# Optimization experiments

Measured on AMD Instinct MI355X. Metric: run time of the kernel, lower is better.

Reference implementation:

```python
import jax, jax.numpy as jnp
import numpy as np

B, L, D, M_MAX = 4, 4096, 1024, 512


def setup_inputs() -> dict:
    key = jax.random.key(0)
    k_ct, k_enc, k_lo, k_hi, k_w = jax.random.split(key, 5)
    concept_tokens = jax.random.normal(k_ct, (B, M_MAX, D), dtype=jnp.float32)
    encoder_out = jax.random.normal(k_enc, (B, L, D), dtype=jnp.float32)
    # sorted unique boundary positions per batch, first boundary at position 0
    rng = np.random.RandomState(0)
    idx = np.stack([np.sort(rng.choice(np.arange(1, L), size=M_MAX - 1, replace=False)) for _ in range(B)])
    boundary_idx = jnp.asarray(np.concatenate([np.zeros((B, 1), dtype=np.int64), idx], axis=1))  # [B, M_max]
    # probs < 0.5 everywhere except at boundary positions (>= 0.5), so cumsum(mask)-1 < M_max
    lo = jax.random.uniform(k_lo, (B, L), minval=0.02, maxval=0.48)
    hi = jax.random.uniform(k_hi, (B, M_MAX), minval=0.5, maxval=1.0)
    rows = jnp.arange(B)[:, None]
    boundary_probs = lo.at[rows, boundary_idx].set(hi)
    concept_mask = jnp.ones((B, M_MAX), dtype=bool)
    W = jax.random.normal(k_w, (D, D), dtype=jnp.float32) * 0.02  # residual_proj.weight (out = x @ W.T)
    return {"concept_tokens": concept_tokens, "encoder_out": encoder_out,
            "boundary_probs": boundary_probs, "boundary_idx": boundary_idx,
            "concept_mask": concept_mask, "W": W}


def _ema_smooth(concept_tokens, p_at_bounds):
    """h_i = (1-p_i)*h_{i-1} + p_i*c_i via associative scan; h_0 = c_0."""
    h0 = concept_tokens[:, 0]                                  # [B, d]
    p_rest = p_at_bounds[:, 1:]                                # [B, M-1]
    decay = jnp.clip(1.0 - p_rest, 1e-7, None)
    b = p_rest[..., None] * concept_tokens[:, 1:]              # [B, M-1, d]
    a = jnp.broadcast_to(decay[..., None], b.shape)

    def combine(x, y):
        a1, b1 = x
        a2, b2 = y
        return a1 * a2, a2 * b1 + b2

    A, Bc = jax.lax.associative_scan(combine, (a, b), axis=1)
    h_rest = A * h0[:, None, :] + Bc                           # h_i = A_i*h0 + B_i
    return jnp.concatenate([h0[:, None, :], h_rest], axis=1)   # [B, M, d]


def reference(concept_tokens, encoder_out, boundary_probs, boundary_idx, concept_mask, W):
    d = encoder_out.shape[-1]
    # Eq.5: EMA over concept tokens with boundary probs gathered at boundary positions
    p_raw = jnp.take_along_axis(boundary_probs, boundary_idx, axis=1)          # [B, M]
    p_at_bounds = jnp.where(concept_mask, p_raw, 1.0)
    p_at_bounds = jnp.clip(p_at_bounds, 0.1, None)
    smoothed = _ema_smooth(concept_tokens, p_at_bounds)                        # [B, M, d]
    # Eq.8: plug-back via running boundary count
    boundary_mask = boundary_probs >= 0.5                                      # [B, L]
    plug_back_idx = jnp.clip(jnp.cumsum(boundary_mask.astype(jnp.int32), axis=1) - 1, 0, None)
    plugback = jnp.take_along_axis(smoothed, plug_back_idx[..., None], axis=1)  # [B, L, d]
    # Eq.6/7/9: confidence + STE (forward value is exactly 1.0)
    b_f = boundary_mask.astype(boundary_probs.dtype)
    c_t = b_f * boundary_probs + (1.0 - b_f) * (1.0 - boundary_probs)
    ste_c = c_t + jax.lax.stop_gradient(1.0 - c_t)
    upsampled = ste_c[..., None] * plugback
    # Eq.3: residual linear (no bias)
    return upsampled + jnp.einsum('bld,ed->ble', encoder_out, W)
```

## Files before the change

kernel.cpp:

```cpp
#include <hip/hip_runtime.h>
#include <hip/hip_bf16.h>
#include <stdint.h>


#define B_  4
#define L_  4096
#define D_  1024
#define M_  512

typedef __attribute__((ext_vector_type(8))) short bf16x8;
typedef __attribute__((ext_vector_type(4))) float f32x4;
typedef __attribute__((ext_vector_type(8))) unsigned short u16x8;

__device__ inline unsigned short f2bf(float f) {
    unsigned u = __float_as_uint(f);
    u += 0x7fffu + ((u >> 16) & 1u);
    return (unsigned short)(u >> 16);
}

__global__ void prep_kernel(const float* __restrict__ enc, const float* __restrict__ W,
                            const float* __restrict__ probs,
                            unsigned short* __restrict__ encb, unsigned short* __restrict__ Wb,
                            int* __restrict__ pbi) {
    __shared__ int part[256];
    int blk = blockIdx.x;
    int tid = threadIdx.x;
    if (blk < 8704) {
        const float* src; unsigned short* dst; int i;
        if (blk < 8192) { src = enc; dst = encb; i = blk * 256 + tid; }
        else            { src = W;   dst = Wb;   i = (blk - 8192) * 256 + tid; }
        float4 x0 = ((const float4*)src)[2 * i];
        float4 x1 = ((const float4*)src)[2 * i + 1];
        u16x8 v;
        v[0] = f2bf(x0.x); v[1] = f2bf(x0.y); v[2] = f2bf(x0.z); v[3] = f2bf(x0.w);
        v[4] = f2bf(x1.x); v[5] = f2bf(x1.y); v[6] = f2bf(x1.z); v[7] = f2bf(x1.w);
        ((u16x8*)dst)[i] = v;
    } else {
        int b = blk - 8704;
        const float4* pr = (const float4*)(probs + b * L_);
        int cnt[16]; int s = 0;
        #pragma unroll
        for (int u = 0; u < 4; ++u) {
            float4 x = pr[tid * 4 + u];
            s += (x.x >= 0.5f); cnt[u * 4 + 0] = s;
            s += (x.y >= 0.5f); cnt[u * 4 + 1] = s;
            s += (x.z >= 0.5f); cnt[u * 4 + 2] = s;
            s += (x.w >= 0.5f); cnt[u * 4 + 3] = s;
        }
        part[tid] = s;
        __syncthreads();
        for (int off = 1; off < 256; off <<= 1) {
            int x = part[tid];
            int y = (tid >= off) ? part[tid - off] : 0;
            __syncthreads();
            part[tid] = x + y;
            __syncthreads();
        }
        int excl = part[tid] - s;
        int4* po = (int4*)(pbi + b * L_ + tid * 16);
        #pragma unroll
        for (int u = 0; u < 4; ++u) {
            int4 o;
            o.x = max(excl + cnt[u * 4 + 0] - 1, 0);
            o.y = max(excl + cnt[u * 4 + 1] - 1, 0);
            o.z = max(excl + cnt[u * 4 + 2] - 1, 0);
            o.w = max(excl + cnt[u * 4 + 3] - 1, 0);
            po[u] = o;
        }
    }
}

__global__ void ema1_kernel(const float* __restrict__ ct, const float* __restrict__ probs,
                            const int* __restrict__ bidx, float2* __restrict__ summ) {
    int b = blockIdx.z, ch = blockIdx.y;
    int d = blockIdx.x * 256 + threadIdx.x;
    __shared__ float pa[64], pb[64];
    if (threadIdx.x < 64) {
        int m = ch * 64 + threadIdx.x;
        int idx = bidx[b * M_ + m];
        float pv = fmaxf(probs[b * L_ + idx], 0.1f);
        pa[threadIdx.x] = (m == 0) ? 0.0f : fmaxf(1.0f - pv, 1e-7f);
        pb[threadIdx.x] = (m == 0) ? 1.0f : pv;
    }
    __syncthreads();
    const float* ctp = ct + ((size_t)b * M_ + ch * 64) * D_ + d;
    float A = 1.0f, Bv = 0.0f;
    #pragma unroll 8
    for (int i = 0; i < 64; ++i) {
        float c = ctp[(size_t)i * D_];
        A  = pa[i] * A;
        Bv = pa[i] * Bv + pb[i] * c;
    }
    summ[((size_t)b * 8 + ch) * D_ + d] = make_float2(A, Bv);
}

__global__ void ema2_kernel(const float* __restrict__ ct, const float* __restrict__ probs,
                            const int* __restrict__ bidx, const float2* __restrict__ summ,
                            float* __restrict__ smoothed) {
    int b = blockIdx.z, ch = blockIdx.y;
    int d = blockIdx.x * 256 + threadIdx.x;
    __shared__ float pa[64], pb[64];
    if (threadIdx.x < 64) {
        int m = ch * 64 + threadIdx.x;
        int idx = bidx[b * M_ + m];
        float pv = fmaxf(probs[b * L_ + idx], 0.1f);
        pa[threadIdx.x] = (m == 0) ? 0.0f : fmaxf(1.0f - pv, 1e-7f);
        pb[threadIdx.x] = (m == 0) ? 1.0f : pv;
    }
    __syncthreads();
    float h = 0.0f;
    for (int c = 0; c < ch; ++c) {
        float2 s2 = summ[((size_t)b * 8 + c) * D_ + d];
        h = s2.x * h + s2.y;
    }
    const float* ctp = ct + ((size_t)b * M_ + ch * 64) * D_ + d;
    float*       smp = smoothed + ((size_t)b * M_ + ch * 64) * D_ + d;
    #pragma unroll 8
    for (int i = 0; i < 64; ++i) {
        float c = ctp[(size_t)i * D_];
        h = pa[i] * h + pb[i] * c;
        smp[(size_t)i * D_] = h;
    }
}

#define NT_ 32

__global__ __launch_bounds__(512, 1) void gemm3_kernel(
    const unsigned short* __restrict__ encb, const unsigned short* __restrict__ Wb,
    const float* __restrict__ smoothed, const int* __restrict__ pbi,
    float* __restrict__ out)
{
    __shared__ __align__(16) unsigned short As[3][256 * 32];
    __shared__ __align__(16) unsigned short Bs[3][256 * 32];

    const int tid  = threadIdx.x;
    const int lane = tid & 63;
    const int w    = tid >> 6;
    const int wm   = w >> 2;
    const int wn   = w & 3;
    const int l15  = lane & 15;
    const int l16  = lane >> 4;

    const int orig = blockIdx.x;
    const int rm   = (orig & 7) * 32 + (orig >> 3);
    const size_t rowBase = (size_t)(rm >> 2) * 256;
    const int    colBase = (rm & 3) * 256;

    const int rsw = (((lane & 3) ^ ((lane >> 2) & 3)) << 3);

#define STAGE(kt, s)                                                                     \
  {                                                                                      \
    _Pragma("unroll")                                                                    \
    for (int i_ = 0; i_ < 2; ++i_) {                                                     \
      int row_ = i_ * 128 + w * 16 + (lane >> 2);                                        \
      const unsigned short* ga_ = encb + (rowBase + row_) * D_ + (kt) * 32 + rsw;        \
      __builtin_amdgcn_global_load_lds(                                                  \
          (const __attribute__((address_space(1))) void*)ga_,                            \
          (__attribute__((address_space(3))) void*)&As[s][i_ * 4096 + w * 512], 16, 0, 0);\
      const unsigned short* gb_ = Wb + (size_t)(colBase + row_) * D_ + (kt) * 32 + rsw;  \
      __builtin_amdgcn_global_load_lds(                                                  \
          (const __attribute__((address_space(1))) void*)gb_,                            \
          (__attribute__((address_space(3))) void*)&Bs[s][i_ * 4096 + w * 512], 16, 0, 0);\
    }                                                                                    \
  }

    f32x4 acc[8][4] = {};

    STAGE(0, 0);
    STAGE(1, 1);
    asm volatile("s_waitcnt vmcnt(4)" ::: "memory");
    __builtin_amdgcn_s_barrier();
    __builtin_amdgcn_sched_barrier(0);

    int s = 0;
    for (int t = 0; t < NT_; ++t) {
        const char* aB = (const char*)As[s];
        const char* bB = (const char*)Bs[s];
        const int swz = (l15 & 3) << 4;
        bf16x8 a[8], bb[4];
        #pragma unroll
        for (int m = 0; m < 8; ++m)
            a[m] = *(const bf16x8*)(aB + (wm * 128 + m * 16 + l15) * 64 + ((l16 * 16) ^ swz));
        #pragma unroll
        for (int n = 0; n < 4; ++n)
            bb[n] = *(const bf16x8*)(bB + (wn * 64 + n * 16 + l15) * 64 + ((l16 * 16) ^ swz));

        int s2 = s + 2; if (s2 >= 3) s2 -= 3;
        if (t + 2 < NT_) STAGE(t + 2, s2);

        __builtin_amdgcn_s_setprio(1);
        #pragma unroll
        for (int m = 0; m < 8; ++m)
            #pragma unroll
            for (int n = 0; n < 4; ++n)
                acc[m][n] = __builtin_amdgcn_mfma_f32_16x16x32_bf16(a[m], bb[n], acc[m][n], 0, 0, 0);
        __builtin_amdgcn_s_setprio(0);

        if (t + 1 < NT_) {
            if (t + 2 < NT_) { asm volatile("s_waitcnt vmcnt(4)" ::: "memory"); }
            else             { asm volatile("s_waitcnt vmcnt(0)" ::: "memory"); }
            __builtin_amdgcn_s_barrier();
            __builtin_amdgcn_sched_barrier(0);
        }
        s += 1; if (s >= 3) s -= 3;
    }
#undef STAGE

    #pragma unroll
    for (int m = 0; m < 8; ++m) {
        const size_t row0 = rowBase + wm * 128 + m * 16;
        #pragma unroll
        for (int j = 0; j < 4; ++j) {
            size_t row = row0 + l16 * 4 + j;
            int b  = (int)(row >> 12);
            int pb = pbi[row];
            pb = pb < (M_ - 1) ? pb : (M_ - 1);
            const float* sm = smoothed + ((size_t)(b * M_ + pb)) * D_;
            #pragma unroll
            for (int n = 0; n < 4; ++n) {
                int col = colBase + wn * 64 + n * 16 + l15;
                out[row * D_ + col] = acc[m][n][j] + sm[col];
            }
        }
    }
}

#define LDP 72
__global__ __launch_bounds__(256, 2) void gemm_fused_kernel(
    const float* __restrict__ enc, const unsigned short* __restrict__ Wb,
    const float* __restrict__ smoothed, const int* __restrict__ pbi,
    float* __restrict__ out)
{
    __shared__ unsigned short Asf[128][LDP];
    __shared__ unsigned short Bsf[128][LDP];
    const int tid  = threadIdx.x;
    const int lane = tid & 63;
    const int wid  = tid >> 6;
    const int wm   = wid >> 1;
    const int wn   = wid & 1;
    const int l15  = lane & 15;
    const int l16  = lane >> 4;
    const size_t rowBase = (size_t)blockIdx.x * 128;
    const int    colBase = blockIdx.y * 128;
    f32x4 acc[4][4] = {};
    for (int t = 0; t < D_ / 64; ++t) {
        const int k0 = t * 64;
        #pragma unroll
        for (int i = 0; i < 4; ++i) {
            int c = i * 256 + tid;
            int r = c >> 3;
            int c8 = c & 7;
            const float4* g = (const float4*)(enc + (rowBase + r) * D_ + k0 + c8 * 8);
            float4 x0 = g[0];
            float4 x1 = g[1];
            u16x8 v;
            v[0] = f2bf(x0.x); v[1] = f2bf(x0.y); v[2] = f2bf(x0.z); v[3] = f2bf(x0.w);
            v[4] = f2bf(x1.x); v[5] = f2bf(x1.y); v[6] = f2bf(x1.z); v[7] = f2bf(x1.w);
            *(u16x8*)&Asf[r][c8 * 8] = v;
        }
        #pragma unroll
        for (int i = 0; i < 4; ++i) {
            int c = i * 256 + tid;
            int r = c >> 3;
            int c8 = c & 7;
            u16x8 v = *(const u16x8*)(Wb + (size_t)(colBase + r) * D_ + k0 + c8 * 8);
            *(u16x8*)&Bsf[r][c8 * 8] = v;
        }
        __syncthreads();
        #pragma unroll
        for (int kk = 0; kk < 2; ++kk) {
            bf16x8 a[4], bbf[4];
            #pragma unroll
            for (int m = 0; m < 4; ++m)
                a[m] = *(const bf16x8*)&Asf[wm * 64 + m * 16 + l15][kk * 32 + l16 * 8];
            #pragma unroll
            for (int n = 0; n < 4; ++n)
                bbf[n] = *(const bf16x8*)&Bsf[wn * 64 + n * 16 + l15][kk * 32 + l16 * 8];
            #pragma unroll
            for (int m = 0; m < 4; ++m)
                #pragma unroll
                for (int n = 0; n < 4; ++n)
                    acc[m][n] = __builtin_amdgcn_mfma_f32_16x16x32_bf16(a[m], bbf[n], acc[m][n], 0, 0, 0);
        }
        __syncthreads();
    }
    #pragma unroll
    for (int m = 0; m < 4; ++m) {
        #pragma unroll
        for (int j = 0; j < 4; ++j) {
            size_t row = rowBase + wm * 64 + m * 16 + l16 * 4 + j;
            int b  = (int)(row >> 12);
            int pb = pbi[row];
            pb = pb < (M_ - 1) ? pb : (M_ - 1);
            const float* sm = smoothed + ((size_t)(b * M_ + pb)) * D_;
            #pragma unroll
            for (int n = 0; n < 4; ++n) {
                int col = colBase + wn * 64 + n * 16 + l15;
                out[row * D_ + col] = acc[m][n][j] + sm[col];
            }
        }
    }
}

extern "C" void kernel_launch(void* const* d_in, const int* in_sizes, int n_in,
                              void* d_out, int out_size, void* d_ws, size_t ws_size,
                              hipStream_t stream) {
    const float* ct    = (const float*)d_in[0];
    const float* enc   = (const float*)d_in[1];
    const float* probs = (const float*)d_in[2];
    const int*   bidx  = (const int*)d_in[3];
    const float* W     = (const float*)d_in[5];
    float* out = (float*)d_out;
    char*  ws  = (char*)d_ws;

    const size_t SZ_ENCB = (size_t)B_ * L_ * D_ * 2;
    const size_t SZ_SM   = (size_t)B_ * M_ * D_ * 4;
    const size_t SZ_PBI  = (size_t)B_ * L_ * 4;
    const size_t SZ_WB   = (size_t)D_ * D_ * 2;
    const size_t SZ_SUMM = (size_t)B_ * 8 * D_ * 8;

    if (ws_size >= SZ_ENCB + SZ_SM + SZ_PBI + SZ_WB + SZ_SUMM) {
        unsigned short* encb     = (unsigned short*)ws;
        float*          smoothed = (float*)(ws + SZ_ENCB);
        int*            pbi      = (int*)(ws + SZ_ENCB + SZ_SM);
        unsigned short* Wb       = (unsigned short*)(ws + SZ_ENCB + SZ_SM + SZ_PBI);
        float2*         summ     = (float2*)(ws + SZ_ENCB + SZ_SM + SZ_PBI + SZ_WB);

        hipLaunchKernelGGL(prep_kernel, dim3(8708), dim3(256), 0, stream,
                           enc, W, probs, encb, Wb, pbi);
        hipLaunchKernelGGL(ema1_kernel, dim3(D_ / 256, 8, B_), dim3(256), 0, stream,
                           ct, probs, bidx, summ);
        hipLaunchKernelGGL(ema2_kernel, dim3(D_ / 256, 8, B_), dim3(256), 0, stream,
                           ct, probs, bidx, summ, smoothed);
        hipLaunchKernelGGL(gemm3_kernel, dim3(256), dim3(512), 0, stream,
                           encb, Wb, smoothed, pbi, out);
    } else {
        float*          smoothed = (float*)ws;
        int*            pbi      = (int*)(ws + SZ_SM);
        unsigned short* Wb       = (unsigned short*)(ws + SZ_SM + SZ_PBI);
        float2*         summ     = (float2*)(ws + SZ_SM + SZ_PBI + SZ_WB);
        hipLaunchKernelGGL(prep_kernel, dim3(8708), dim3(256), 0, stream,
                           enc, W, probs, (unsigned short*)summ , Wb, pbi);
        hipLaunchKernelGGL(ema1_kernel, dim3(D_ / 256, 8, B_), dim3(256), 0, stream,
                           ct, probs, bidx, summ);
        hipLaunchKernelGGL(ema2_kernel, dim3(D_ / 256, 8, B_), dim3(256), 0, stream,
                           ct, probs, bidx, summ, smoothed);
        hipLaunchKernelGGL(gemm_fused_kernel, dim3(B_ * L_ / 128, D_ / 128), dim3(256), 0, stream,
                           enc, Wb, smoothed, pbi, out);
    }
}
```

Measured before the change: 177.3 us.

## Fuse conversion, boundary scan and two-pass EMA into one prep kernel

Merges the bf16 conversion, plug-back index prefix scan and the two EMA kernels into a single launch with 512-thread blocks. The EMA chunk-summary combine now happens in shared memory inside one block per (batch, 64-column slice) instead of through a global workspace and a second kernel. This removes two kernel launches and the global summary round trip, but puts the EMA's serial chunk scan inside the same grid as the bandwidth-bound conversion blocks.

```diff
diff --git a/kernel.cpp b/kernel.cpp
--- a/kernel.cpp
+++ b/kernel.cpp
@@ -18,48 +18,54 @@
     return (unsigned short)(u >> 16);
 }
 
-__global__ void prep_kernel(const float* __restrict__ enc, const float* __restrict__ W,
-                            const float* __restrict__ probs,
-                            unsigned short* __restrict__ encb, unsigned short* __restrict__ Wb,
-                            int* __restrict__ pbi) {
-    __shared__ int part[256];
-    int blk = blockIdx.x;
-    int tid = threadIdx.x;
-    if (blk < 8704) {
-        const float* src; unsigned short* dst; int i;
-        if (blk < 8192) { src = enc; dst = encb; i = blk * 256 + tid; }
-        else            { src = W;   dst = Wb;   i = (blk - 8192) * 256 + tid; }
+__global__ void prep_all_kernel(const float* __restrict__ enc, const float* __restrict__ W,
+                                const float* __restrict__ probs, const float* __restrict__ ct,
+                                const int* __restrict__ bidx,
+                                unsigned short* __restrict__ encb, unsigned short* __restrict__ Wb,
+                                int* __restrict__ pbi, float* __restrict__ smoothed,
+                                int encBlocks) {
+    __shared__ int part[512];
+    __shared__ float ad[M_], bdp[M_];
+    __shared__ float Ac[8][64], Bc[8][64], Hin[8][64];
+
+    const int blk = blockIdx.x;
+    const int t   = threadIdx.x;
+
+    if (blk < encBlocks + 256) {
+        const float* src; unsigned short* dst; size_t i;
+        if (blk < encBlocks) { src = enc; dst = encb; i = (size_t)blk * 512 + t; }
+        else                 { src = W;   dst = Wb;   i = (size_t)(blk - encBlocks) * 512 + t; }
         float4 x0 = ((const float4*)src)[2 * i];
         float4 x1 = ((const float4*)src)[2 * i + 1];
         u16x8 v;
         v[0] = f2bf(x0.x); v[1] = f2bf(x0.y); v[2] = f2bf(x0.z); v[3] = f2bf(x0.w);
         v[4] = f2bf(x1.x); v[5] = f2bf(x1.y); v[6] = f2bf(x1.z); v[7] = f2bf(x1.w);
         ((u16x8*)dst)[i] = v;
-    } else {
-        int b = blk - 8704;
+    } else if (blk < encBlocks + 260) {
+        int b = blk - (encBlocks + 256);
         const float4* pr = (const float4*)(probs + b * L_);
-        int cnt[16]; int s = 0;
-        #pragma unroll
-        for (int u = 0; u < 4; ++u) {
-            float4 x = pr[tid * 4 + u];
+        int cnt[8]; int s = 0;
+        #pragma unroll
+        for (int u = 0; u < 2; ++u) {
+            float4 x = pr[t * 2 + u];
             s += (x.x >= 0.5f); cnt[u * 4 + 0] = s;
             s += (x.y >= 0.5f); cnt[u * 4 + 1] = s;
             s += (x.z >= 0.5f); cnt[u * 4 + 2] = s;
             s += (x.w >= 0.5f); cnt[u * 4 + 3] = s;
         }
-        part[tid] = s;
-        __syncthreads();
-        for (int off = 1; off < 256; off <<= 1) {
-            int x = part[tid];
-            int y = (tid >= off) ? part[tid - off] : 0;
+        part[t] = s;
+        __syncthreads();
+        for (int off = 1; off < 512; off <<= 1) {
+            int x = part[t];
+            int y = (t >= off) ? part[t - off] : 0;
             __syncthreads();
-            part[tid] = x + y;
+            part[t] = x + y;
             __syncthreads();
         }
-        int excl = part[tid] - s;
-        int4* po = (int4*)(pbi + b * L_ + tid * 16);
-        #pragma unroll
-        for (int u = 0; u < 4; ++u) {
+        int excl = part[t] - s;
+        int4* po = (int4*)(pbi + b * L_ + t * 8);
+        #pragma unroll
+        for (int u = 0; u < 2; ++u) {
             int4 o;
             o.x = max(excl + cnt[u * 4 + 0] - 1, 0);
             o.y = max(excl + cnt[u * 4 + 1] - 1, 0);
@@ -67,59 +73,49 @@
             o.w = max(excl + cnt[u * 4 + 3] - 1, 0);
             po[u] = o;
         }
-    }
-}
-
-__global__ void ema1_kernel(const float* __restrict__ ct, const float* __restrict__ probs,
-                            const int* __restrict__ bidx, float2* __restrict__ summ) {
-    int b = blockIdx.z, ch = blockIdx.y;
-    int d = blockIdx.x * 256 + threadIdx.x;
-    __shared__ float pa[64], pb[64];
-    if (threadIdx.x < 64) {
-        int m = ch * 64 + threadIdx.x;
-        int idx = bidx[b * M_ + m];
-        float pv = fmaxf(probs[b * L_ + idx], 0.1f);
-        pa[threadIdx.x] = (m == 0) ? 0.0f : fmaxf(1.0f - pv, 1e-7f);
-        pb[threadIdx.x] = (m == 0) ? 1.0f : pv;
-    }
-    __syncthreads();
-    const float* ctp = ct + ((size_t)b * M_ + ch * 64) * D_ + d;
-    float A = 1.0f, Bv = 0.0f;
-    #pragma unroll 8
-    for (int i = 0; i < 64; ++i) {
-        float c = ctp[(size_t)i * D_];
-        A  = pa[i] * A;
-        Bv = pa[i] * Bv + pb[i] * c;
-    }
-    summ[((size_t)b * 8 + ch) * D_ + d] = make_float2(A, Bv);
-}
-
-__global__ void ema2_kernel(const float* __restrict__ ct, const float* __restrict__ probs,
-                            const int* __restrict__ bidx, const float2* __restrict__ summ,
-                            float* __restrict__ smoothed) {
-    int b = blockIdx.z, ch = blockIdx.y;
-    int d = blockIdx.x * 256 + threadIdx.x;
-    __shared__ float pa[64], pb[64];
-    if (threadIdx.x < 64) {
-        int m = ch * 64 + threadIdx.x;
-        int idx = bidx[b * M_ + m];
-        float pv = fmaxf(probs[b * L_ + idx], 0.1f);
-        pa[threadIdx.x] = (m == 0) ? 0.0f : fmaxf(1.0f - pv, 1e-7f);
-        pb[threadIdx.x] = (m == 0) ? 1.0f : pv;
-    }
-    __syncthreads();
-    float h = 0.0f;
-    for (int c = 0; c < ch; ++c) {
-        float2 s2 = summ[((size_t)b * 8 + c) * D_ + d];
-        h = s2.x * h + s2.y;
-    }
-    const float* ctp = ct + ((size_t)b * M_ + ch * 64) * D_ + d;
-    float*       smp = smoothed + ((size_t)b * M_ + ch * 64) * D_ + d;
-    #pragma unroll 8
-    for (int i = 0; i < 64; ++i) {
-        float c = ctp[(size_t)i * D_];
-        h = pa[i] * h + pb[i] * c;
-        smp[(size_t)i * D_] = h;
+    } else {
+        int idx = blk - (encBlocks + 260);
+        int b  = idx >> 4;
+        int d0 = (idx & 15) * 64;
+        int dl = t & 63;
+        int ch = t >> 6;
+        {
+            int m = t;
+            int bi = bidx[b * M_ + m];
+            float p = fmaxf(probs[b * L_ + bi], 0.1f);
+            ad[m]  = (m == 0) ? 0.0f : fmaxf(1.0f - p, 1e-7f);
+            bdp[m] = (m == 0) ? 1.0f : p;
+        }
+        __syncthreads();
+        const float* ctp = ct + ((size_t)b * M_ + ch * 64) * D_ + d0 + dl;
+        float A = 1.0f, Bv = 0.0f;
+        #pragma unroll 8
+        for (int i = 0; i < 64; ++i) {
+            int m = ch * 64 + i;
+            float c = ctp[(size_t)i * D_];
+            A  = ad[m] * A;
+            Bv = ad[m] * Bv + bdp[m] * c;
+        }
+        Ac[ch][dl] = A; Bc[ch][dl] = Bv;
+        __syncthreads();
+        if (t < 64) {
+            float H = 0.0f;
+            #pragma unroll
+            for (int c = 0; c < 8; ++c) {
+                Hin[c][t] = H;
+                H = Ac[c][t] * H + Bc[c][t];
+            }
+        }
+        __syncthreads();
+        float h = Hin[ch][dl];
+        float* smp = smoothed + ((size_t)b * M_ + ch * 64) * D_ + d0 + dl;
+        #pragma unroll 8
+        for (int i = 0; i < 64; ++i) {
+            int m = ch * 64 + i;
+            float c = ctp[(size_t)i * D_];
+            h = ad[m] * h + bdp[m] * c;
+            smp[(size_t)i * D_] = h;
+        }
     }
 }
 
@@ -317,34 +313,26 @@
     const size_t SZ_SM   = (size_t)B_ * M_ * D_ * 4;
     const size_t SZ_PBI  = (size_t)B_ * L_ * 4;
     const size_t SZ_WB   = (size_t)D_ * D_ * 2;
-    const size_t SZ_SUMM = (size_t)B_ * 8 * D_ * 8;
-
-    if (ws_size >= SZ_ENCB + SZ_SM + SZ_PBI + SZ_WB + SZ_SUMM) {
+
+    if (ws_size >= SZ_ENCB + SZ_SM + SZ_PBI + SZ_WB) {
         unsigned short* encb     = (unsigned short*)ws;
         float*          smoothed = (float*)(ws + SZ_ENCB);
         int*            pbi      = (int*)(ws + SZ_ENCB + SZ_SM);
         unsigned short* Wb       = (unsigned short*)(ws + SZ_ENCB + SZ_SM + SZ_PBI);
-        float2*         summ     = (float2*)(ws + SZ_ENCB + SZ_SM + SZ_PBI + SZ_WB);
-
-        hipLaunchKernelGGL(prep_kernel, dim3(8708), dim3(256), 0, stream,
-                           enc, W, probs, encb, Wb, pbi);
-        hipLaunchKernelGGL(ema1_kernel, dim3(D_ / 256, 8, B_), dim3(256), 0, stream,
-                           ct, probs, bidx, summ);
-        hipLaunchKernelGGL(ema2_kernel, dim3(D_ / 256, 8, B_), dim3(256), 0, stream,
-                           ct, probs, bidx, summ, smoothed);
+
+        const int encBlocks = B_ * L_ * D_ / 4096;
+        const int nBlocks   = encBlocks + 256 + B_ + B_ * D_ / 64;
+        hipLaunchKernelGGL(prep_all_kernel, dim3(nBlocks), dim3(512), 0, stream,
+                           enc, W, probs, ct, bidx, encb, Wb, pbi, smoothed, encBlocks);
         hipLaunchKernelGGL(gemm3_kernel, dim3(256), dim3(512), 0, stream,
                            encb, Wb, smoothed, pbi, out);
     } else {
         float*          smoothed = (float*)ws;
         int*            pbi      = (int*)(ws + SZ_SM);
         unsigned short* Wb       = (unsigned short*)(ws + SZ_SM + SZ_PBI);
-        float2*         summ     = (float2*)(ws + SZ_SM + SZ_PBI + SZ_WB);
-        hipLaunchKernelGGL(prep_kernel, dim3(8708), dim3(256), 0, stream,
-                           enc, W, probs, (unsigned short*)summ , Wb, pbi);
-        hipLaunchKernelGGL(ema1_kernel, dim3(D_ / 256, 8, B_), dim3(256), 0, stream,
-                           ct, probs, bidx, summ);
-        hipLaunchKernelGGL(ema2_kernel, dim3(D_ / 256, 8, B_), dim3(256), 0, stream,
-                           ct, probs, bidx, summ, smoothed);
+        const int nBlocks = 0 + 256 + B_ + B_ * D_ / 64;
+        hipLaunchKernelGGL(prep_all_kernel, dim3(nBlocks), dim3(512), 0, stream,
+                           enc, W, probs, ct, bidx, (unsigned short*)ws , Wb, pbi, smoothed, 0);
         hipLaunchKernelGGL(gemm_fused_kernel, dim3(B_ * L_ / 128, D_ / 128), dim3(256), 0, stream,
                            enc, Wb, smoothed, pbi, out);
     }
```

Result: faster. 171.1 us (-3.5%).
